# Kernel tuning notes

Measured on AMD Instinct MI355X. Metric: run time of the kernel, lower is better.

## Reference

```python
import jax, jax.numpy as jnp
import numpy as np


def setup_inputs() -> dict:
    key = jax.random.key(0)
    ks = jax.random.split(key, 9)
    N, C, H, W, K = 8, 512, 64, 64, 32
    C4 = C // 4
    s = lambda k, shape, scale=0.02: jax.random.normal(k, shape, dtype=jnp.float32) * scale
    return {
        "x": jax.random.normal(ks[0], (N, C, H, W), dtype=jnp.float32),
        "y": jax.random.normal(ks[1], (N, K, C), dtype=jnp.float32),
        "wq": s(ks[2], (C4, C)),
        "bq": s(ks[3], (C4,)),
        "wk": s(ks[4], (C4, C)),
        "bk": s(ks[5], (C4,)),
        "wv": s(ks[6], (C, C)),
        "bv": s(ks[7], (C,)),
        "scale": s(ks[8], (1,), 1.0),
    }


def reference(x, y, wq, bq, wk, bk, wv, bv, scale):
    N, C, H, W = x.shape
    # 1x1 conv query: (N,C,H,W) -> (N,C4,H,W) -> (N, HW, C4)
    q = jnp.einsum('nchw,oc->nhwo', x, wq) + bq  # (N,H,W,C4)
    q = q.reshape(N, H * W, -1)                   # (N, HW, C4)
    # key/value linears on centers y: (N,K,C)
    k = y @ wk.T + bk                             # (N, K, C4)
    v = y @ wv.T + bv                             # (N, K, C)
    energy = jnp.einsum('npc,nkc->npk', q, k)     # (N, HW, K)
    attn = jax.nn.softmax(energy, axis=-1)
    out = jnp.einsum('nkc,npk->ncp', v, attn)     # (N, C, HW)
    out = out.reshape(N, C, H, W)
    return scale[0] * out + x
```

## Files before the change

### kernel.cpp

```cpp
#include <hip/hip_runtime.h>


#define N_  8
#define C_  512
#define HW_ 4096
#define K_  32

typedef __attribute__((ext_vector_type(8))) short bf16x8;
typedef __attribute__((ext_vector_type(4))) float f32x4;
typedef __attribute__((ext_vector_type(4))) unsigned short u16x4;
typedef __attribute__((ext_vector_type(4))) int i32x4;

__device__ __forceinline__ unsigned short f2b(float f) {
    union { float f; unsigned u; } v; v.f = f;
    unsigned r = v.u + 0x7FFFu + ((v.u >> 16) & 1u);
    return (unsigned short)(r >> 16);
}
__device__ __forceinline__ float b2f(unsigned short h) {
    union { unsigned u; float f; } v; v.u = ((unsigned)h) << 16; return v.f;
}
__device__ __forceinline__ int cvtpk(float a, float b) {
    int r;
    asm("v_cvt_pk_bf16_f32 %0, %1, %2" : "=v"(r) : "v"(a), "v"(b));
    return r;
}

__device__ __forceinline__ int wqk_idx(int kk, int c) {
    return ((((c >> 5) * 2 + (kk >> 4)) * 64 + ((c >> 3) & 3) * 16 + (kk & 15)) << 3) + (c & 7);
}

__global__ __launch_bounds__(256) void prep_kernel(
    const float* __restrict__ y, const float* __restrict__ wq, const float* __restrict__ bq,
    const float* __restrict__ wk, const float* __restrict__ bk,
    const float* __restrict__ wv, const float* __restrict__ bv,
    unsigned short* __restrict__ wqkf, float* __restrict__ bqk, unsigned short* __restrict__ vtf)
{
    const int bid = blockIdx.x;
    const int t = threadIdx.x;

    if (bid < 256) {
        __shared__ float vred[3][4][16][8];
        const int n   = bid >> 5;
        const int ct  = bid & 31;
        const int cl  = t & 15;
        const int kko = (t >> 4) & 3;
        const int jq4 = t >> 6;
        const int c   = ct * 16 + cl;

        const float* yb  = y  + ((size_t)n * K_ + kko * 8) * C_ + jq4 * 128;
        const float* wvb = wv + (size_t)c * C_ + jq4 * 128;
        float acc[8] = {0,0,0,0,0,0,0,0};
        #pragma unroll 4
        for (int jj = 0; jj < 32; ++jj) {
            float4 w4 = *(const float4*)(wvb + jj * 4);
            #pragma unroll
            for (int u = 0; u < 8; ++u) {
                float4 y4 = *(const float4*)(yb + (size_t)u * C_ + jj * 4);
                acc[u] += y4.x * w4.x + y4.y * w4.y + y4.z * w4.z + y4.w * w4.w;
            }
        }
        if (jq4 > 0) {
            #pragma unroll
            for (int u = 0; u < 8; ++u) vred[jq4 - 1][kko][cl][u] = acc[u];
        }
        __syncthreads();
        if (jq4 == 0) {
            const float bvc = bv[c];
            unsigned short o[8];
            #pragma unroll
            for (int u = 0; u < 8; ++u) {
                float s = acc[u] + vred[0][kko][cl][u] + vred[1][kko][cl][u]
                        + vred[2][kko][cl][u] + bvc;
                o[u] = f2b(s);
            }
            i32x4 pk = { (int)(o[0] | ((unsigned)o[1] << 16)), (int)(o[2] | ((unsigned)o[3] << 16)),
                         (int)(o[4] | ((unsigned)o[5] << 16)), (int)(o[6] | ((unsigned)o[7] << 16)) };
            *(i32x4*)(vtf + (size_t)n * (K_ * C_) + (size_t)((ct * 64 + kko * 16 + cl) * 8)) = pk;
        }
    } else {
        __shared__ __align__(16) float kp[2][128];
        __shared__ __align__(16) float kr[128];
        const int b = bid - 256;
        const int n = b >> 5, kk = b & 31;
        const int o = t & 127, half = t >> 7;

        const float* yb  = y  + ((size_t)n * K_ + kk) * C_ + half * 256;
        const float* wkb = wk + (size_t)o * C_ + half * 256;
        float a = 0.f;
        #pragma unroll 4
        for (int jq = 0; jq < 64; ++jq) {
            float4 w4 = *(const float4*)(wkb + jq * 4);
            float4 y4 = *(const float4*)(yb + jq * 4);
            a += y4.x * w4.x + y4.y * w4.y + y4.z * w4.z + y4.w * w4.w;
        }
        kp[half][o] = a;
        __syncthreads();
        if (t < 128) kr[t] = kp[0][t] + kp[1][t] + bk[t];
        __syncthreads();
        if (t < 64) {
            float s = kr[t] * bq[t] + kr[t + 64] * bq[t + 64];
            #pragma unroll
            for (int d = 32; d > 0; d >>= 1) s += __shfl_down(s, d);
            if (t == 0) bqk[n * K_ + kk] = s;
        }
        const int c1 = t, c2 = t + 256;
        float s1 = 0.f, s2 = 0.f;
        for (int oq = 0; oq < 32; ++oq) {
            float4 k4 = *(const float4*)(&kr[oq * 4]);
            const float* wq0 = wq + (size_t)(oq * 4) * C_;
            s1 += k4.x * wq0[c1] + k4.y * wq0[C_ + c1] + k4.z * wq0[2*C_ + c1] + k4.w * wq0[3*C_ + c1];
            s2 += k4.x * wq0[c2] + k4.y * wq0[C_ + c2] + k4.z * wq0[2*C_ + c2] + k4.w * wq0[3*C_ + c2];
        }
        unsigned short* wqf_n = wqkf + (size_t)n * (K_ * C_);
        wqf_n[wqk_idx(kk, c1)] = f2b(s1);
        wqf_n[wqk_idx(kk, c2)] = f2b(s2);
    }
}

__global__ __launch_bounds__(256) void main_kernel(
    const float* __restrict__ x, const unsigned short* __restrict__ wqkf,
    const unsigned short* __restrict__ vtf, const float* __restrict__ bqk,
    const float* __restrict__ scale, float* __restrict__ out)
{
    __shared__ __align__(16) unsigned short xl[2][16384];
    __shared__ float e_lds[32][36];

    const int swz = (blockIdx.x & 7) * 64 + (blockIdx.x >> 3);
    const int n    = swz >> 6;
    const int pair = swz & 63;
    const int t  = threadIdx.x;
    const int w  = t >> 6, l = t & 63;
    const int l15 = l & 15, lg = l >> 4;
    const float* xg = x + (size_t)n * C_ * HW_;
    float* og = out + (size_t)n * C_ * HW_;
    const unsigned short* wqf  = wqkf + (size_t)n * (K_ * C_);
    const unsigned short* vtfn = vtf  + (size_t)n * (K_ * C_);

    const int mh = w;
    const int kt = w >> 1;
    const int pt = w & 1;
    const int px = t & 31, g = t >> 5;
    const float fs = scale[0];
    const float bq_ = bqk[n * K_ + kt * 16 + l15];

    bf16x8 vf[8];
    #pragma unroll
    for (int mi = 0; mi < 8; ++mi)
        vf[mi] = *(const bf16x8*)(vtfn + ((size_t)(mh * 8 + mi) * 64 + l) * 8);

    {
        const float* xc = xg + pair * 64 + px;
        float r[4][8];
        #pragma unroll
        for (int h = 0; h < 2; ++h) {
            #pragma unroll
            for (int u = 0; u < 4; ++u)
                #pragma unroll
                for (int j = 0; j < 8; ++j)
                    r[u][j] = xc[(size_t)(g * 8 + (h * 4 + u) * 64 + j) * HW_];
            #pragma unroll
            for (int u = 0; u < 4; ++u) {
                const int cbase = g * 8 + (h * 4 + u) * 64;
                const int elem = ((cbase >> 5) * 1024) + (((cbase >> 3) & 3) * 256) + px * 8;
                i32x4 pk = { cvtpk(r[u][0], r[u][1]), cvtpk(r[u][2], r[u][3]),
                             cvtpk(r[u][4], r[u][5]), cvtpk(r[u][6], r[u][7]) };
                *(i32x4*)(&xl[0][elem]) = pk;
            }
        }
    }
    __syncthreads();

    for (int i = 0; i < 2; ++i) {
        const unsigned short* xb = xl[i];
        unsigned short* xw = xl[1 - i];
        const float* xcn = xg + pair * 64 + 32 + px;
        float rs[4][8];

        if (i == 0) {
            #pragma unroll
            for (int u = 0; u < 4; ++u)
                #pragma unroll
                for (int j = 0; j < 8; ++j)
                    rs[u][j] = xcn[(size_t)(g * 8 + u * 64 + j) * HW_];
        }

        {
            bf16x8 b0 = *(const bf16x8*)(wqf + ((size_t)(0 * 2 + kt) * 64 + l) * 8);
            bf16x8 b1 = *(const bf16x8*)(wqf + ((size_t)(1 * 2 + kt) * 64 + l) * 8);
            f32x4 acc = {0.f, 0.f, 0.f, 0.f};
            const unsigned short* xbase = xb + lg * 256 + (pt * 16 + l15) * 8;
            for (int cs = 0; cs < 16; ++cs) {
                bf16x8 b2;
                if (cs < 14) b2 = *(const bf16x8*)(wqf + ((size_t)((cs + 2) * 2 + kt) * 64 + l) * 8);
                const bf16x8 af = *(const bf16x8*)(xbase + cs * 1024);
                acc = __builtin_amdgcn_mfma_f32_16x16x32_bf16(af, b0, acc, 0, 0, 0);
                b0 = b1; b1 = b2;
            }
            #pragma unroll
            for (int r = 0; r < 4; ++r)
                e_lds[pt * 16 + lg * 4 + r][kt * 16 + l15] = acc[r] + bq_;
        }

        if (i == 0) {
            #pragma unroll
            for (int u = 0; u < 4; ++u) {
                const int cbase = g * 8 + u * 64;
                const int elem = ((cbase >> 5) * 1024) + (((cbase >> 3) & 3) * 256) + px * 8;
                i32x4 pk = { cvtpk(rs[u][0], rs[u][1]), cvtpk(rs[u][2], rs[u][3]),
                             cvtpk(rs[u][4], rs[u][5]), cvtpk(rs[u][6], rs[u][7]) };
                *(i32x4*)(&xw[elem]) = pk;
            }
            #pragma unroll
            for (int u = 0; u < 4; ++u)
                #pragma unroll
                for (int j = 0; j < 8; ++j)
                    rs[u][j] = xcn[(size_t)(g * 8 + (u + 4) * 64 + j) * HW_];
        }
        __syncthreads();

        bf16x8 paf0, paf1;
        {
            float e0[32], e1[32];
            #pragma unroll
            for (int q = 0; q < 8; ++q) {
                float4 q0 = *(const float4*)&e_lds[l15][4 * q];
                float4 q1 = *(const float4*)&e_lds[16 + l15][4 * q];
                e0[4*q] = q0.x; e0[4*q+1] = q0.y; e0[4*q+2] = q0.z; e0[4*q+3] = q0.w;
                e1[4*q] = q1.x; e1[4*q+1] = q1.y; e1[4*q+2] = q1.z; e1[4*q+3] = q1.w;
            }
            float m0 = e0[0], m1 = e1[0];
            #pragma unroll
            for (int k = 1; k < 32; ++k) { m0 = fmaxf(m0, e0[k]); m1 = fmaxf(m1, e1[k]); }
            float s0 = 0.f, s1 = 0.f;
            #pragma unroll
            for (int k = 0; k < 32; ++k) {
                e0[k] = __expf(e0[k] - m0); s0 += e0[k];
                e1[k] = __expf(e1[k] - m1); s1 += e1[k];
            }
            const float i0 = 1.f / s0, i1 = 1.f / s1;
            union { int q[4]; bf16x8 v; } u0, u1;
            #pragma unroll
            for (int jj = 0; jj < 4; ++jj) {
                u0.q[jj] = cvtpk(e0[8*lg + 2*jj] * i0, e0[8*lg + 2*jj + 1] * i0);
                u1.q[jj] = cvtpk(e1[8*lg + 2*jj] * i1, e1[8*lg + 2*jj + 1] * i1);
            }
            paf0 = u0.v; paf1 = u1.v;
        }

        {
            const int p0i = pair * 64 + i * 32;
            const int pxa = p0i + l15, pxb = p0i + 16 + l15;
            const int mt0 = mh * 8;
            #pragma unroll
            for (int mi = 0; mi < 8; ++mi) {
                const int mt = mt0 + mi;
                f32x4 d0 = __builtin_amdgcn_mfma_f32_16x16x32_bf16(vf[mi], paf0, (f32x4){0.f,0.f,0.f,0.f}, 0, 0, 0);
                f32x4 d1 = __builtin_amdgcn_mfma_f32_16x16x32_bf16(vf[mi], paf1, (f32x4){0.f,0.f,0.f,0.f}, 0, 0, 0);
                const int base = (mt >> 1) * 1024 + ((2 * mt + (lg >> 1)) & 3) * 256 + (lg & 1) * 4;
                const u16x4 ra = *(const u16x4*)(xb + base + l15 * 8);
                const u16x4 rb = *(const u16x4*)(xb + base + (16 + l15) * 8);
                const int cc = mt * 16 + lg * 4;
                #pragma unroll
                for (int r = 0; r < 4; ++r) {
                    og[(size_t)(cc + r) * HW_ + pxa] = fs * d0[r] + b2f(ra[r]);
                    og[(size_t)(cc + r) * HW_ + pxb] = fs * d1[r] + b2f(rb[r]);
                }
            }
        }

        if (i == 0) {
            #pragma unroll
            for (int u = 0; u < 4; ++u) {
                const int cbase = g * 8 + (u + 4) * 64;
                const int elem = ((cbase >> 5) * 1024) + (((cbase >> 3) & 3) * 256) + px * 8;
                i32x4 pk = { cvtpk(rs[u][0], rs[u][1]), cvtpk(rs[u][2], rs[u][3]),
                             cvtpk(rs[u][4], rs[u][5]), cvtpk(rs[u][6], rs[u][7]) };
                *(i32x4*)(&xw[elem]) = pk;
            }
        }
        __syncthreads();
    }
}

extern "C" void kernel_launch(void* const* d_in, const int* in_sizes, int n_in,
                              void* d_out, int out_size, void* d_ws, size_t ws_size,
                              hipStream_t stream) {
    const float* x     = (const float*)d_in[0];
    const float* y     = (const float*)d_in[1];
    const float* wq    = (const float*)d_in[2];
    const float* bq    = (const float*)d_in[3];
    const float* wk    = (const float*)d_in[4];
    const float* bk    = (const float*)d_in[5];
    const float* wv    = (const float*)d_in[6];
    const float* bv    = (const float*)d_in[7];
    const float* scale = (const float*)d_in[8];

    unsigned short* wqkf = (unsigned short*)d_ws;
    unsigned short* vtf  = wqkf + (size_t)N_ * K_ * C_;
    float* bqk = (float*)((char*)d_ws + 524288);

    prep_kernel<<<512, 256, 0, stream>>>(y, wq, bq, wk, bk, wv, bv, wqkf, bqk, vtf);
    main_kernel<<<512, 256, 0, stream>>>(x, wqkf, vtf, bqk, scale, (float*)d_out);
}
```

Before: 64.32 us.

## Split main kernel into producer and consumer warps for x tile loading

Main kernel blocks grow to 512 threads. Four producer waves load and convert the x tiles to bf16 in LDS, while four consumer waves do the energy MFMA, softmax and output MFMA. The goal is to overlap the global load of the second tile with compute on the first without holding staged registers in the compute waves. It also unrolls the prep kernel's wq projection loop. The cost is doubled threads per block, which may lower occupancy, and producer waves that sit idle in the second iteration.

```diff
diff --git a/kernel.cpp b/kernel.cpp
--- a/kernel.cpp
+++ b/kernel.cpp
@@ -105,6 +105,7 @@
         }
         const int c1 = t, c2 = t + 256;
         float s1 = 0.f, s2 = 0.f;
+        #pragma unroll 8
         for (int oq = 0; oq < 32; ++oq) {
             float4 k4 = *(const float4*)(&kr[oq * 4]);
             const float* wq0 = wq + (size_t)(oq * 4) * C_;
@@ -117,7 +118,7 @@
     }
 }
 
-__global__ __launch_bounds__(256) void main_kernel(
+__global__ __launch_bounds__(512) void main_kernel(
     const float* __restrict__ x, const unsigned short* __restrict__ wqkf,
     const unsigned short* __restrict__ vtf, const float* __restrict__ bqk,
     const float* __restrict__ scale, float* __restrict__ out)
@@ -125,10 +126,11 @@
     __shared__ __align__(16) unsigned short xl[2][16384];
     __shared__ float e_lds[32][36];
 
-    const int swz = (blockIdx.x & 7) * 64 + (blockIdx.x >> 3);
-    const int n    = swz >> 6;
-    const int pair = swz & 63;
+    const int blk = (blockIdx.x & 7) * 64 + (blockIdx.x >> 3);
+    const int n     = blk >> 6;
+    const int tile0 = (blk & 63) * 2;
     const int t  = threadIdx.x;
+    const bool producer = (t >= 256);
     const int w  = t >> 6, l = t & 63;
     const int l15 = l & 15, lg = l >> 4;
     const float* xg = x + (size_t)n * C_ * HW_;
@@ -136,23 +138,27 @@
     const unsigned short* wqf  = wqkf + (size_t)n * (K_ * C_);
     const unsigned short* vtfn = vtf  + (size_t)n * (K_ * C_);
 
-    const int mh = w;
-    const int kt = w >> 1;
+    const int mh = w & 3;
+    const int kt = (w & 3) >> 1;
     const int pt = w & 1;
-    const int px = t & 31, g = t >> 5;
     const float fs = scale[0];
-    const float bq_ = bqk[n * K_ + kt * 16 + l15];
-
+    float bq_ = 0.f;
     bf16x8 vf[8];
-    #pragma unroll
-    for (int mi = 0; mi < 8; ++mi)
-        vf[mi] = *(const bf16x8*)(vtfn + ((size_t)(mh * 8 + mi) * 64 + l) * 8);
-
-    {
-        const float* xc = xg + pair * 64 + px;
-        float r[4][8];
+    if (!producer) {
+        bq_ = bqk[n * K_ + kt * 16 + l15];
+        #pragma unroll
+        for (int mi = 0; mi < 8; ++mi)
+            vf[mi] = *(const bf16x8*)(vtfn + ((size_t)(mh * 8 + mi) * 64 + l) * 8);
+    }
+
+    const int tp = t & 255;
+    const int px = tp & 31, g = tp >> 5;
+
+    if (producer) {
+        const float* xc = xg + tile0 * 32 + px;
         #pragma unroll
         for (int h = 0; h < 2; ++h) {
+            float r[4][8];
             #pragma unroll
             for (int u = 0; u < 4; ++u)
                 #pragma unroll
@@ -171,20 +177,10 @@
     __syncthreads();
 
     for (int i = 0; i < 2; ++i) {
+        const int p0i = (tile0 + i) * 32;
         const unsigned short* xb = xl[i];
-        unsigned short* xw = xl[1 - i];
-        const float* xcn = xg + pair * 64 + 32 + px;
-        float rs[4][8];
-
-        if (i == 0) {
-            #pragma unroll
-            for (int u = 0; u < 4; ++u)
-                #pragma unroll
-                for (int j = 0; j < 8; ++j)
-                    rs[u][j] = xcn[(size_t)(g * 8 + u * 64 + j) * HW_];
-        }
-
-        {
+
+        if (!producer) {
             bf16x8 b0 = *(const bf16x8*)(wqf + ((size_t)(0 * 2 + kt) * 64 + l) * 8);
             bf16x8 b1 = *(const bf16x8*)(wqf + ((size_t)(1 * 2 + kt) * 64 + l) * 8);
             f32x4 acc = {0.f, 0.f, 0.f, 0.f};
@@ -200,55 +196,59 @@
             for (int r = 0; r < 4; ++r)
                 e_lds[pt * 16 + lg * 4 + r][kt * 16 + l15] = acc[r] + bq_;
         }
-
-        if (i == 0) {
-            #pragma unroll
-            for (int u = 0; u < 4; ++u) {
-                const int cbase = g * 8 + u * 64;
-                const int elem = ((cbase >> 5) * 1024) + (((cbase >> 3) & 3) * 256) + px * 8;
-                i32x4 pk = { cvtpk(rs[u][0], rs[u][1]), cvtpk(rs[u][2], rs[u][3]),
-                             cvtpk(rs[u][4], rs[u][5]), cvtpk(rs[u][6], rs[u][7]) };
-                *(i32x4*)(&xw[elem]) = pk;
-            }
-            #pragma unroll
-            for (int u = 0; u < 4; ++u)
-                #pragma unroll
-                for (int j = 0; j < 8; ++j)
-                    rs[u][j] = xcn[(size_t)(g * 8 + (u + 4) * 64 + j) * HW_];
-        }
-        __syncthreads();
-
-        bf16x8 paf0, paf1;
-        {
-            float e0[32], e1[32];
-            #pragma unroll
-            for (int q = 0; q < 8; ++q) {
-                float4 q0 = *(const float4*)&e_lds[l15][4 * q];
-                float4 q1 = *(const float4*)&e_lds[16 + l15][4 * q];
-                e0[4*q] = q0.x; e0[4*q+1] = q0.y; e0[4*q+2] = q0.z; e0[4*q+3] = q0.w;
-                e1[4*q] = q1.x; e1[4*q+1] = q1.y; e1[4*q+2] = q1.z; e1[4*q+3] = q1.w;
-            }
-            float m0 = e0[0], m1 = e1[0];
-            #pragma unroll
-            for (int k = 1; k < 32; ++k) { m0 = fmaxf(m0, e0[k]); m1 = fmaxf(m1, e1[k]); }
-            float s0 = 0.f, s1 = 0.f;
-            #pragma unroll
-            for (int k = 0; k < 32; ++k) {
-                e0[k] = __expf(e0[k] - m0); s0 += e0[k];
-                e1[k] = __expf(e1[k] - m1); s1 += e1[k];
-            }
-            const float i0 = 1.f / s0, i1 = 1.f / s1;
-            union { int q[4]; bf16x8 v; } u0, u1;
-            #pragma unroll
-            for (int jj = 0; jj < 4; ++jj) {
-                u0.q[jj] = cvtpk(e0[8*lg + 2*jj] * i0, e0[8*lg + 2*jj + 1] * i0);
-                u1.q[jj] = cvtpk(e1[8*lg + 2*jj] * i1, e1[8*lg + 2*jj + 1] * i1);
-            }
-            paf0 = u0.v; paf1 = u1.v;
-        }
-
-        {
-            const int p0i = pair * 64 + i * 32;
+        __syncthreads();
+
+        if (producer) {
+            if (i == 0) {
+                const float* xc = xg + (tile0 + 1) * 32 + px;
+                #pragma unroll
+                for (int h = 0; h < 2; ++h) {
+                    float r[4][8];
+                    #pragma unroll
+                    for (int u = 0; u < 4; ++u)
+                        #pragma unroll
+                        for (int j = 0; j < 8; ++j)
+                            r[u][j] = xc[(size_t)(g * 8 + (h * 4 + u) * 64 + j) * HW_];
+                    #pragma unroll
+                    for (int u = 0; u < 4; ++u) {
+                        const int cbase = g * 8 + (h * 4 + u) * 64;
+                        const int elem = ((cbase >> 5) * 1024) + (((cbase >> 3) & 3) * 256) + px * 8;
+                        i32x4 pk = { cvtpk(r[u][0], r[u][1]), cvtpk(r[u][2], r[u][3]),
+                                     cvtpk(r[u][4], r[u][5]), cvtpk(r[u][6], r[u][7]) };
+                        *(i32x4*)(&xl[1][elem]) = pk;
+                    }
+                }
+            }
+        } else {
+            bf16x8 paf0, paf1;
+            {
+                float e0[32], e1[32];
+                #pragma unroll
+                for (int q = 0; q < 8; ++q) {
+                    float4 q0 = *(const float4*)&e_lds[l15][4 * q];
+                    float4 q1 = *(const float4*)&e_lds[16 + l15][4 * q];
+                    e0[4*q] = q0.x; e0[4*q+1] = q0.y; e0[4*q+2] = q0.z; e0[4*q+3] = q0.w;
+                    e1[4*q] = q1.x; e1[4*q+1] = q1.y; e1[4*q+2] = q1.z; e1[4*q+3] = q1.w;
+                }
+                float m0 = e0[0], m1 = e1[0];
+                #pragma unroll
+                for (int k = 1; k < 32; ++k) { m0 = fmaxf(m0, e0[k]); m1 = fmaxf(m1, e1[k]); }
+                float s0 = 0.f, s1 = 0.f;
+                #pragma unroll
+                for (int k = 0; k < 32; ++k) {
+                    e0[k] = __expf(e0[k] - m0); s0 += e0[k];
+                    e1[k] = __expf(e1[k] - m1); s1 += e1[k];
+                }
+                const float i0 = 1.f / s0, i1 = 1.f / s1;
+                union { int q[4]; bf16x8 v; } u0, u1;
+                #pragma unroll
+                for (int jj = 0; jj < 4; ++jj) {
+                    u0.q[jj] = cvtpk(e0[8*lg + 2*jj] * i0, e0[8*lg + 2*jj + 1] * i0);
+                    u1.q[jj] = cvtpk(e1[8*lg + 2*jj] * i1, e1[8*lg + 2*jj + 1] * i1);
+                }
+                paf0 = u0.v; paf1 = u1.v;
+            }
+
             const int pxa = p0i + l15, pxb = p0i + 16 + l15;
             const int mt0 = mh * 8;
             #pragma unroll
@@ -265,17 +265,6 @@
                     og[(size_t)(cc + r) * HW_ + pxa] = fs * d0[r] + b2f(ra[r]);
                     og[(size_t)(cc + r) * HW_ + pxb] = fs * d1[r] + b2f(rb[r]);
                 }
-            }
-        }
-
-        if (i == 0) {
-            #pragma unroll
-            for (int u = 0; u < 4; ++u) {
-                const int cbase = g * 8 + (u + 4) * 64;
-                const int elem = ((cbase >> 5) * 1024) + (((cbase >> 3) & 3) * 256) + px * 8;
-                i32x4 pk = { cvtpk(rs[u][0], rs[u][1]), cvtpk(rs[u][2], rs[u][3]),
-                             cvtpk(rs[u][4], rs[u][5]), cvtpk(rs[u][6], rs[u][7]) };
-                *(i32x4*)(&xw[elem]) = pk;
             }
         }
         __syncthreads();
@@ -300,5 +289,5 @@
     float* bqk = (float*)((char*)d_ws + 524288);
 
     prep_kernel<<<512, 256, 0, stream>>>(y, wq, bq, wk, bk, wv, bv, wqkf, bqk, vtf);
-    main_kernel<<<512, 256, 0, stream>>>(x, wqkf, vtf, bqk, scale, (float*)d_out);
-}
+    main_kernel<<<512, 512, 0, stream>>>(x, wqkf, vtf, bqk, scale, (float*)d_out);
+}
```

Result: slower. 91.89 us (+42.9%).

## Single-buffer x tile in LDS, split loads across query GEMM, re-read residual in fp32

Applied to the files above, without the earlier changes.

Cuts the LDS x buffer from two tiles to one, which frees shared memory and may allow more resident blocks per CU. Each half-tile's global loads are now interleaved with half of the query-projection MFMA loop, and the next tile's loads overlap the output phase. The residual is re-read from global memory in full fp32 with a software prefetch, instead of being taken from the bf16 LDS copy. This improves residual accuracy but adds extra global reads of x and more barriers.

```diff
diff --git a/kernel.cpp b/kernel.cpp
--- a/kernel.cpp
+++ b/kernel.cpp
@@ -8,7 +8,6 @@
 
 typedef __attribute__((ext_vector_type(8))) short bf16x8;
 typedef __attribute__((ext_vector_type(4))) float f32x4;
-typedef __attribute__((ext_vector_type(4))) unsigned short u16x4;
 typedef __attribute__((ext_vector_type(4))) int i32x4;
 
 __device__ __forceinline__ unsigned short f2b(float f) {
@@ -16,9 +15,6 @@
     unsigned r = v.u + 0x7FFFu + ((v.u >> 16) & 1u);
     return (unsigned short)(r >> 16);
 }
-__device__ __forceinline__ float b2f(unsigned short h) {
-    union { unsigned u; float f; } v; v.u = ((unsigned)h) << 16; return v.f;
-}
 __device__ __forceinline__ int cvtpk(float a, float b) {
     int r;
     asm("v_cvt_pk_bf16_f32 %0, %1, %2" : "=v"(r) : "v"(a), "v"(b));
@@ -27,6 +23,64 @@
 
 __device__ __forceinline__ int wqk_idx(int kk, int c) {
     return ((((c >> 5) * 2 + (kk >> 4)) * 64 + ((c >> 3) & 3) * 16 + (kk & 15)) << 3) + (c & 7);
+}
+
+__device__ __forceinline__ void load_half(const float* xc, int h, int g, float r[4][8]) {
+    #pragma unroll
+    for (int u = 0; u < 4; ++u)
+        #pragma unroll
+        for (int j = 0; j < 8; ++j)
+            r[u][j] = xc[(size_t)(g * 8 + (h * 4 + u) * 64 + j) * HW_];
+}
+__device__ __forceinline__ void write_half(unsigned short* xl, int h, int g, int px, float r[4][8]) {
+    #pragma unroll
+    for (int u = 0; u < 4; ++u) {
+        const int cbase = g * 8 + (h * 4 + u) * 64;
+        const int elem = ((cbase >> 5) * 1024) + (((cbase >> 3) & 3) * 256) + px * 8;
+        i32x4 pk = { cvtpk(r[u][0], r[u][1]), cvtpk(r[u][2], r[u][3]),
+                     cvtpk(r[u][4], r[u][5]), cvtpk(r[u][6], r[u][7]) };
+        *(i32x4*)(xl + elem) = pk;
+    }
+}
+__device__ __forceinline__ void p1_range(const unsigned short* xl, const unsigned short* wqf,
+                                         int kt, int pt, int l, int l15, int lg,
+                                         int cs0, int cs1, f32x4& acc, bf16x8& b0, bf16x8& b1) {
+    const unsigned short* xbase = xl + lg * 256 + (pt * 16 + l15) * 8;
+    for (int cs = cs0; cs < cs1; ++cs) {
+        bf16x8 b2;
+        if (cs < 14) b2 = *(const bf16x8*)(wqf + ((size_t)((cs + 2) * 2 + kt) * 64 + l) * 8);
+        const bf16x8 af = *(const bf16x8*)(xbase + cs * 1024);
+        acc = __builtin_amdgcn_mfma_f32_16x16x32_bf16(af, b0, acc, 0, 0, 0);
+        b0 = b1; b1 = b2;
+    }
+}
+__device__ __forceinline__ void softmax2(const float (*e_lds)[36], int l15, int lg,
+                                         bf16x8& paf0, bf16x8& paf1) {
+    float e0[32], e1[32];
+    #pragma unroll
+    for (int q = 0; q < 8; ++q) {
+        float4 q0 = *(const float4*)&e_lds[l15][4 * q];
+        float4 q1 = *(const float4*)&e_lds[16 + l15][4 * q];
+        e0[4*q] = q0.x; e0[4*q+1] = q0.y; e0[4*q+2] = q0.z; e0[4*q+3] = q0.w;
+        e1[4*q] = q1.x; e1[4*q+1] = q1.y; e1[4*q+2] = q1.z; e1[4*q+3] = q1.w;
+    }
+    float m0 = e0[0], m1 = e1[0];
+    #pragma unroll
+    for (int k = 1; k < 32; ++k) { m0 = fmaxf(m0, e0[k]); m1 = fmaxf(m1, e1[k]); }
+    float s0 = 0.f, s1 = 0.f;
+    #pragma unroll
+    for (int k = 0; k < 32; ++k) {
+        e0[k] = __expf(e0[k] - m0); s0 += e0[k];
+        e1[k] = __expf(e1[k] - m1); s1 += e1[k];
+    }
+    const float i0 = 1.f / s0, i1 = 1.f / s1;
+    union { int q[4]; bf16x8 v; } u0, u1;
+    #pragma unroll
+    for (int jj = 0; jj < 4; ++jj) {
+        u0.q[jj] = cvtpk(e0[8*lg + 2*jj] * i0, e0[8*lg + 2*jj + 1] * i0);
+        u1.q[jj] = cvtpk(e1[8*lg + 2*jj] * i1, e1[8*lg + 2*jj + 1] * i1);
+    }
+    paf0 = u0.v; paf1 = u1.v;
 }
 
 __global__ __launch_bounds__(256) void prep_kernel(
@@ -122,12 +176,13 @@
     const unsigned short* __restrict__ vtf, const float* __restrict__ bqk,
     const float* __restrict__ scale, float* __restrict__ out)
 {
-    __shared__ __align__(16) unsigned short xl[2][16384];
+    __shared__ __align__(16) unsigned short xl[16384];
     __shared__ float e_lds[32][36];
 
     const int swz = (blockIdx.x & 7) * 64 + (blockIdx.x >> 3);
-    const int n    = swz >> 6;
-    const int pair = swz & 63;
+    const int n   = swz >> 6;
+    const int p00 = (swz & 63) * 64;
+    const int p01 = p00 + 32;
     const int t  = threadIdx.x;
     const int w  = t >> 6, l = t & 63;
     const int l15 = l & 15, lg = l >> 4;
@@ -142,6 +197,8 @@
     const int px = t & 31, g = t >> 5;
     const float fs = scale[0];
     const float bq_ = bqk[n * K_ + kt * 16 + l15];
+    const float* xc0 = xg + p00 + px;
+    const float* xc1 = xg + p01 + px;
 
     bf16x8 vf[8];
     #pragma unroll
@@ -149,136 +206,124 @@
         vf[mi] = *(const bf16x8*)(vtfn + ((size_t)(mh * 8 + mi) * 64 + l) * 8);
 
     {
-        const float* xc = xg + pair * 64 + px;
         float r[4][8];
-        #pragma unroll
-        for (int h = 0; h < 2; ++h) {
-            #pragma unroll
-            for (int u = 0; u < 4; ++u)
-                #pragma unroll
-                for (int j = 0; j < 8; ++j)
-                    r[u][j] = xc[(size_t)(g * 8 + (h * 4 + u) * 64 + j) * HW_];
-            #pragma unroll
-            for (int u = 0; u < 4; ++u) {
-                const int cbase = g * 8 + (h * 4 + u) * 64;
-                const int elem = ((cbase >> 5) * 1024) + (((cbase >> 3) & 3) * 256) + px * 8;
-                i32x4 pk = { cvtpk(r[u][0], r[u][1]), cvtpk(r[u][2], r[u][3]),
-                             cvtpk(r[u][4], r[u][5]), cvtpk(r[u][6], r[u][7]) };
-                *(i32x4*)(&xl[0][elem]) = pk;
-            }
-        }
-    }
-    __syncthreads();
-
-    for (int i = 0; i < 2; ++i) {
-        const unsigned short* xb = xl[i];
-        unsigned short* xw = xl[1 - i];
-        const float* xcn = xg + pair * 64 + 32 + px;
-        float rs[4][8];
-
-        if (i == 0) {
-            #pragma unroll
-            for (int u = 0; u < 4; ++u)
-                #pragma unroll
-                for (int j = 0; j < 8; ++j)
-                    rs[u][j] = xcn[(size_t)(g * 8 + u * 64 + j) * HW_];
-        }
-
+        load_half(xc0, 0, g, r);
+        write_half(xl, 0, g, px, r);
+    }
+    __syncthreads();
+    f32x4 acc = {0.f, 0.f, 0.f, 0.f};
+    bf16x8 b0 = *(const bf16x8*)(wqf + ((size_t)(0 * 2 + kt) * 64 + l) * 8);
+    bf16x8 b1 = *(const bf16x8*)(wqf + ((size_t)(1 * 2 + kt) * 64 + l) * 8);
+    {
+        float r[4][8];
+        load_half(xc0, 1, g, r);
+        p1_range(xl, wqf, kt, pt, l, l15, lg, 0, 8, acc, b0, b1);
+        write_half(xl, 1, g, px, r);
+    }
+    __syncthreads();
+    p1_range(xl, wqf, kt, pt, l, l15, lg, 8, 16, acc, b0, b1);
+    #pragma unroll
+    for (int r = 0; r < 4; ++r)
+        e_lds[pt * 16 + lg * 4 + r][kt * 16 + l15] = acc[r] + bq_;
+    __syncthreads();
+
+    {
+        bf16x8 paf0, paf1;
+        softmax2(e_lds, l15, lg, paf0, paf1);
+
+        float rst[4][8];
+        load_half(xc1, 0, g, rst);
+
+        const int pxa = p00 + l15, pxb = p00 + 16 + l15;
+        const int mt0 = mh * 8;
+        float xr0[4], xr1[4];
         {
-            bf16x8 b0 = *(const bf16x8*)(wqf + ((size_t)(0 * 2 + kt) * 64 + l) * 8);
-            bf16x8 b1 = *(const bf16x8*)(wqf + ((size_t)(1 * 2 + kt) * 64 + l) * 8);
-            f32x4 acc = {0.f, 0.f, 0.f, 0.f};
-            const unsigned short* xbase = xb + lg * 256 + (pt * 16 + l15) * 8;
-            for (int cs = 0; cs < 16; ++cs) {
-                bf16x8 b2;
-                if (cs < 14) b2 = *(const bf16x8*)(wqf + ((size_t)((cs + 2) * 2 + kt) * 64 + l) * 8);
-                const bf16x8 af = *(const bf16x8*)(xbase + cs * 1024);
-                acc = __builtin_amdgcn_mfma_f32_16x16x32_bf16(af, b0, acc, 0, 0, 0);
-                b0 = b1; b1 = b2;
-            }
-            #pragma unroll
-            for (int r = 0; r < 4; ++r)
-                e_lds[pt * 16 + lg * 4 + r][kt * 16 + l15] = acc[r] + bq_;
-        }
-
-        if (i == 0) {
-            #pragma unroll
-            for (int u = 0; u < 4; ++u) {
-                const int cbase = g * 8 + u * 64;
-                const int elem = ((cbase >> 5) * 1024) + (((cbase >> 3) & 3) * 256) + px * 8;
-                i32x4 pk = { cvtpk(rs[u][0], rs[u][1]), cvtpk(rs[u][2], rs[u][3]),
-                             cvtpk(rs[u][4], rs[u][5]), cvtpk(rs[u][6], rs[u][7]) };
-                *(i32x4*)(&xw[elem]) = pk;
-            }
-            #pragma unroll
-            for (int u = 0; u < 4; ++u)
-                #pragma unroll
-                for (int j = 0; j < 8; ++j)
-                    rs[u][j] = xcn[(size_t)(g * 8 + (u + 4) * 64 + j) * HW_];
-        }
-        __syncthreads();
-
-        bf16x8 paf0, paf1;
-        {
-            float e0[32], e1[32];
-            #pragma unroll
-            for (int q = 0; q < 8; ++q) {
-                float4 q0 = *(const float4*)&e_lds[l15][4 * q];
-                float4 q1 = *(const float4*)&e_lds[16 + l15][4 * q];
-                e0[4*q] = q0.x; e0[4*q+1] = q0.y; e0[4*q+2] = q0.z; e0[4*q+3] = q0.w;
-                e1[4*q] = q1.x; e1[4*q+1] = q1.y; e1[4*q+2] = q1.z; e1[4*q+3] = q1.w;
-            }
-            float m0 = e0[0], m1 = e1[0];
-            #pragma unroll
-            for (int k = 1; k < 32; ++k) { m0 = fmaxf(m0, e0[k]); m1 = fmaxf(m1, e1[k]); }
-            float s0 = 0.f, s1 = 0.f;
-            #pragma unroll
-            for (int k = 0; k < 32; ++k) {
-                e0[k] = __expf(e0[k] - m0); s0 += e0[k];
-                e1[k] = __expf(e1[k] - m1); s1 += e1[k];
-            }
-            const float i0 = 1.f / s0, i1 = 1.f / s1;
-            union { int q[4]; bf16x8 v; } u0, u1;
-            #pragma unroll
-            for (int jj = 0; jj < 4; ++jj) {
-                u0.q[jj] = cvtpk(e0[8*lg + 2*jj] * i0, e0[8*lg + 2*jj + 1] * i0);
-                u1.q[jj] = cvtpk(e1[8*lg + 2*jj] * i1, e1[8*lg + 2*jj + 1] * i1);
-            }
-            paf0 = u0.v; paf1 = u1.v;
-        }
-
-        {
-            const int p0i = pair * 64 + i * 32;
-            const int pxa = p0i + l15, pxb = p0i + 16 + l15;
-            const int mt0 = mh * 8;
-            #pragma unroll
-            for (int mi = 0; mi < 8; ++mi) {
-                const int mt = mt0 + mi;
-                f32x4 d0 = __builtin_amdgcn_mfma_f32_16x16x32_bf16(vf[mi], paf0, (f32x4){0.f,0.f,0.f,0.f}, 0, 0, 0);
-                f32x4 d1 = __builtin_amdgcn_mfma_f32_16x16x32_bf16(vf[mi], paf1, (f32x4){0.f,0.f,0.f,0.f}, 0, 0, 0);
-                const int base = (mt >> 1) * 1024 + ((2 * mt + (lg >> 1)) & 3) * 256 + (lg & 1) * 4;
-                const u16x4 ra = *(const u16x4*)(xb + base + l15 * 8);
-                const u16x4 rb = *(const u16x4*)(xb + base + (16 + l15) * 8);
-                const int cc = mt * 16 + lg * 4;
+            const int c0 = mt0 * 16 + lg * 4;
+            #pragma unroll
+            for (int r = 0; r < 4; ++r) {
+                xr0[r] = xg[(size_t)(c0 + r) * HW_ + pxa];
+                xr1[r] = xg[(size_t)(c0 + r) * HW_ + pxb];
+            }
+        }
+        for (int mi = 0; mi < 8; ++mi) {
+            const int mt = mt0 + mi;
+            float y0[4], y1[4];
+            if (mi < 7) {
+                const int cn = (mt + 1) * 16 + lg * 4;
                 #pragma unroll
                 for (int r = 0; r < 4; ++r) {
-                    og[(size_t)(cc + r) * HW_ + pxa] = fs * d0[r] + b2f(ra[r]);
-                    og[(size_t)(cc + r) * HW_ + pxb] = fs * d1[r] + b2f(rb[r]);
+                    y0[r] = xg[(size_t)(cn + r) * HW_ + pxa];
+                    y1[r] = xg[(size_t)(cn + r) * HW_ + pxb];
                 }
             }
-        }
-
-        if (i == 0) {
-            #pragma unroll
-            for (int u = 0; u < 4; ++u) {
-                const int cbase = g * 8 + (u + 4) * 64;
-                const int elem = ((cbase >> 5) * 1024) + (((cbase >> 3) & 3) * 256) + px * 8;
-                i32x4 pk = { cvtpk(rs[u][0], rs[u][1]), cvtpk(rs[u][2], rs[u][3]),
-                             cvtpk(rs[u][4], rs[u][5]), cvtpk(rs[u][6], rs[u][7]) };
-                *(i32x4*)(&xw[elem]) = pk;
-            }
-        }
-        __syncthreads();
+            f32x4 d0 = __builtin_amdgcn_mfma_f32_16x16x32_bf16(vf[mi], paf0, (f32x4){0.f,0.f,0.f,0.f}, 0, 0, 0);
+            f32x4 d1 = __builtin_amdgcn_mfma_f32_16x16x32_bf16(vf[mi], paf1, (f32x4){0.f,0.f,0.f,0.f}, 0, 0, 0);
+            const int cc = mt * 16 + lg * 4;
+            #pragma unroll
+            for (int r = 0; r < 4; ++r) {
+                og[(size_t)(cc + r) * HW_ + pxa] = fs * d0[r] + xr0[r];
+                og[(size_t)(cc + r) * HW_ + pxb] = fs * d1[r] + xr1[r];
+            }
+            #pragma unroll
+            for (int r = 0; r < 4; ++r) { xr0[r] = y0[r]; xr1[r] = y1[r]; }
+        }
+        write_half(xl, 0, g, px, rst);
+    }
+    __syncthreads();
+
+    acc = (f32x4){0.f, 0.f, 0.f, 0.f};
+    b0 = *(const bf16x8*)(wqf + ((size_t)(0 * 2 + kt) * 64 + l) * 8);
+    b1 = *(const bf16x8*)(wqf + ((size_t)(1 * 2 + kt) * 64 + l) * 8);
+    {
+        float r[4][8];
+        load_half(xc1, 1, g, r);
+        p1_range(xl, wqf, kt, pt, l, l15, lg, 0, 8, acc, b0, b1);
+        write_half(xl, 1, g, px, r);
+    }
+    __syncthreads();
+    p1_range(xl, wqf, kt, pt, l, l15, lg, 8, 16, acc, b0, b1);
+    #pragma unroll
+    for (int r = 0; r < 4; ++r)
+        e_lds[pt * 16 + lg * 4 + r][kt * 16 + l15] = acc[r] + bq_;
+    __syncthreads();
+
+    {
+        bf16x8 paf0, paf1;
+        softmax2(e_lds, l15, lg, paf0, paf1);
+
+        const int pxa = p01 + l15, pxb = p01 + 16 + l15;
+        const int mt0 = mh * 8;
+        float xr0[4], xr1[4];
+        {
+            const int c0 = mt0 * 16 + lg * 4;
+            #pragma unroll
+            for (int r = 0; r < 4; ++r) {
+                xr0[r] = xg[(size_t)(c0 + r) * HW_ + pxa];
+                xr1[r] = xg[(size_t)(c0 + r) * HW_ + pxb];
+            }
+        }
+        for (int mi = 0; mi < 8; ++mi) {
+            const int mt = mt0 + mi;
+            float y0[4], y1[4];
+            if (mi < 7) {
+                const int cn = (mt + 1) * 16 + lg * 4;
+                #pragma unroll
+                for (int r = 0; r < 4; ++r) {
+                    y0[r] = xg[(size_t)(cn + r) * HW_ + pxa];
+                    y1[r] = xg[(size_t)(cn + r) * HW_ + pxb];
+                }
+            }
+            f32x4 d0 = __builtin_amdgcn_mfma_f32_16x16x32_bf16(vf[mi], paf0, (f32x4){0.f,0.f,0.f,0.f}, 0, 0, 0);
+            f32x4 d1 = __builtin_amdgcn_mfma_f32_16x16x32_bf16(vf[mi], paf1, (f32x4){0.f,0.f,0.f,0.f}, 0, 0, 0);
+            const int cc = mt * 16 + lg * 4;
+            #pragma unroll
+            for (int r = 0; r < 4; ++r) {
+                og[(size_t)(cc + r) * HW_ + pxa] = fs * d0[r] + xr0[r];
+                og[(size_t)(cc + r) * HW_ + pxb] = fs * d1[r] + xr1[r];
+            }
+            #pragma unroll
+            for (int r = 0; r < 4; ++r) { xr0[r] = y0[r]; xr1[r] = y1[r]; }
+        }
     }
 }
 
```

Result: slower. 79.46 us (+23.5%).
